# Kernel tuning notes

Hardware: AMD Instinct MI355X
Metric: run time of the kernel (lower is better)

## Reference

```python
import jax, jax.numpy as jnp
import numpy as np

HIDDEN = 2048
NUM_HEADS = 16
HEAD_DIM = 128
WINDOW = 1024
ROPE_THETA = 10000.0
B, L = 1, 4096


def setup_inputs() -> dict:
    key = jax.random.key(0)
    k0, k1, k2, k3, k4 = jax.random.split(key, 5)
    s = 1.0 / np.sqrt(HIDDEN)
    return {
        "hidden_states": jax.random.normal(k0, (B, L, HIDDEN), dtype=jnp.float32),
        "wq": jax.random.normal(k1, (HIDDEN, NUM_HEADS * HEAD_DIM), dtype=jnp.float32) * s,
        "wk": jax.random.normal(k2, (HIDDEN, NUM_HEADS * HEAD_DIM), dtype=jnp.float32) * s,
        "wv": jax.random.normal(k3, (HIDDEN, NUM_HEADS * HEAD_DIM), dtype=jnp.float32) * s,
        "wo": jax.random.normal(k4, (NUM_HEADS * HEAD_DIM, HIDDEN), dtype=jnp.float32) * s,
    }


def _apply_rotary(x, cos, sin):
    # x: [B, H, L, D]; cos/sin: [L, D/2]
    d2 = x.shape[-1] // 2
    x1, x2 = x[..., :d2], x[..., d2:]
    return jnp.concatenate([x1 * cos - x2 * sin, x2 * cos + x1 * sin], axis=-1)


def reference(hidden_states, wq, wk, wv, wo):
    Bsz, Ln, _ = hidden_states.shape
    dtype = hidden_states.dtype
    scale = HEAD_DIM ** (-0.5)

    def split_heads(x):
        return x.reshape(Bsz, Ln, NUM_HEADS, HEAD_DIM).transpose(0, 2, 1, 3)

    q = split_heads(hidden_states @ wq)
    k = split_heads(hidden_states @ wk)
    v = split_heads(hidden_states @ wv)

    inv_freq = 1.0 / (ROPE_THETA ** (jnp.arange(0, HEAD_DIM, 2, dtype=jnp.float32) / HEAD_DIM))
    pos = jnp.arange(Ln, dtype=jnp.float32)
    freqs = pos[:, None] * inv_freq[None, :]  # [L, D/2]
    cos = jnp.cos(freqs).astype(dtype)
    sin = jnp.sin(freqs).astype(dtype)

    q = _apply_rotary(q, cos, sin)
    k = _apply_rotary(k, cos, sin)

    q_pos = jnp.arange(Ln)[:, None]
    k_pos = jnp.arange(Ln)[None, :]
    valid = (k_pos > q_pos - WINDOW) & (k_pos <= q_pos)  # [L, L]
    neg = jnp.finfo(dtype).min

    attn = jnp.einsum("bhqd,bhkd->bhqk", q, k) * scale
    attn = jnp.where(valid, attn, neg)
    attn = jax.nn.softmax(attn, axis=-1)
    out = jnp.einsum("bhqk,bhkd->bhqd", attn, v)
    out = out.transpose(0, 2, 1, 3).reshape(Bsz, Ln, NUM_HEADS * HEAD_DIM)
    return out @ wo
```

## Files before the change

kernel.cpp:

```cpp
#include <hip/hip_runtime.h>
#include <cstdint>
#include <cstddef>

typedef unsigned short u16;
typedef __bf16 bf16x8 __attribute__((ext_vector_type(8)));
typedef float f32x4 __attribute__((ext_vector_type(4)));
typedef unsigned short u16x8 __attribute__((ext_vector_type(8)));

#define SEQ 4096
#define HID 2048
#define NH 16
#define HD 128
#define WIN 1024

__device__ __forceinline__ float bf2f(u16 u) {
  union { unsigned int i; float f; } v; v.i = ((unsigned int)u) << 16; return v.f;
}
__device__ __forceinline__ u16 f2bf(float f) {
  union { float f; unsigned int i; } v; v.f = f;
  unsigned int r = v.i + 0x7FFFu + ((v.i >> 16) & 1u);
  return (u16)(r >> 16);
}
__device__ __forceinline__ u16 f2bf_rne(float f) {
  union { __bf16 b; u16 u; } v; v.b = (__bf16)f; return v.u;
}
__device__ __forceinline__ unsigned pk2(float lo, float hi) {
  return (unsigned)f2bf_rne(lo) | ((unsigned)f2bf_rne(hi) << 16);
}
__device__ __forceinline__ float exp2a(float x) {
  float r; asm("v_exp_f32 %0, %1" : "=v"(r) : "v"(x)); return r;
}
template<int L2R>
__device__ __forceinline__ unsigned swz(unsigned o) { return o ^ (((o >> L2R) & 7u) << 4); }

__device__ __forceinline__ void gload_lds16(const u16* g, u16* l) {
  __builtin_amdgcn_global_load_lds((const __attribute__((address_space(1))) void*)g,
                                   (__attribute__((address_space(3))) void*)l, 16, 0, 0);
}


__global__ void cast_f32_bf16(const float* __restrict__ in, u16* __restrict__ out, int n4) {
  int i = blockIdx.x * blockDim.x + threadIdx.x;
  if (i < n4) {
    float4 v = ((const float4*)in)[i];
    union { u16 u[4]; unsigned long long ll; } r;
    r.u[0] = f2bf(v.x); r.u[1] = f2bf(v.y); r.u[2] = f2bf(v.z); r.u[3] = f2bf(v.w);
    ((unsigned long long*)out)[i] = r.ll;
  }
}

__global__ void transpose_cast4(const float* __restrict__ w0, const float* __restrict__ w1,
                                const float* __restrict__ w2, const float* __restrict__ w3,
                                u16* __restrict__ o0, u16* __restrict__ o1,
                                u16* __restrict__ o2, u16* __restrict__ o3) {
  __shared__ float t[32][33];
  const float* W = (blockIdx.z == 0) ? w0 : (blockIdx.z == 1) ? w1 : (blockIdx.z == 2) ? w2 : w3;
  u16* Wt = (blockIdx.z == 0) ? o0 : (blockIdx.z == 1) ? o1 : (blockIdx.z == 2) ? o2 : o3;
  const int tx = threadIdx.x & 31, ty = threadIdx.x >> 5;
  const int x0 = blockIdx.x * 32, y0 = blockIdx.y * 32;
#pragma unroll
  for (int i = 0; i < 4; ++i)
    t[ty + i * 8][tx] = W[(size_t)(y0 + ty + i * 8) * HID + x0 + tx];
  __syncthreads();
#pragma unroll
  for (int i = 0; i < 4; ++i)
    Wt[(size_t)(x0 + ty + i * 8) * HID + y0 + tx] = f2bf(t[tx][ty + i * 8]);
}

__global__ void rope_table(float* __restrict__ ctab, float* __restrict__ stab) {
  int idx = blockIdx.x * blockDim.x + threadIdx.x;
  int pos = idx >> 6, i = idx & 63;
  float invf = expf(-(float)i * 0.14391156831212787f);
  float ang = (float)pos * invf;
  float s, c;
  sincosf(ang, &s, &c);
  ctab[idx] = c; stab[idx] = s;
}


__global__ __launch_bounds__(256, 2) void gemm_qkv_kernel(
    const u16* __restrict__ X, const u16* __restrict__ Wqt, const u16* __restrict__ Wkt,
    const u16* __restrict__ Wvt, u16* __restrict__ Qo, u16* __restrict__ Ko, u16* __restrict__ Vo,
    const float* __restrict__ ctab, const float* __restrict__ stab) {
  __shared__ u16 ldsA[2][8192];
  __shared__ u16 ldsB[2][8192];
  int flat = (blockIdx.z * 32 + blockIdx.y) * 16 + blockIdx.x;
  int nf = (flat & 7) * 192 + (flat >> 3);
  int bx = nf & 15, by = (nf >> 4) & 31, bz = nf >> 9;
  const u16* Bt = (bz == 0) ? Wqt : (bz == 1) ? Wkt : Wvt;
  u16* Cp = (bz == 0) ? Qo : (bz == 1) ? Ko : Vo;
  const int brow = by * 128, bcol = bx * 128;

  const int lane = threadIdx.x & 63;
  const int wv = threadIdx.x >> 6;
  const int g = lane >> 4, c = lane & 15;
  const int K = HID, N = HID;

  const f32x4 zero = {0.f, 0.f, 0.f, 0.f};
  f32x4 acc[2][8];
#pragma unroll
  for (int m = 0; m < 2; ++m)
#pragma unroll
    for (int n = 0; n < 8; ++n) acc[m][n] = zero;

  auto stage = [&](int buf, int kt) {
    const int k0 = kt * 64;
#pragma unroll
    for (int i = 0; i < 4; ++i) {
      unsigned o = ((unsigned)(wv * 4 + i) * 64 + (unsigned)lane) * 16u;
      unsigned r = o >> 7;
      unsigned cb = swz<7>(o) & 127u;
      const size_t gcol = (size_t)k0 + (cb >> 1);
      gload_lds16(X + (size_t)(brow + r) * K + gcol, &ldsA[buf][(wv * 4 + i) * 512]);
      gload_lds16(Bt + (size_t)(bcol + r) * K + gcol, &ldsB[buf][(wv * 4 + i) * 512]);
    }
  };

  stage(0, 0);
  __syncthreads();
  int buf = 0;
  const int nt = K / 64;
  for (int kt = 0; kt < nt; ++kt) {
    if (kt + 1 < nt) stage(buf ^ 1, kt + 1);
    __builtin_amdgcn_s_setprio(1);
#pragma unroll
    for (int s = 0; s < 2; ++s) {
      const unsigned kb = (unsigned)(s * 64 + g * 16);
      bf16x8 af[2], bfv[8];
#pragma unroll
      for (int m = 0; m < 2; ++m) {
        unsigned row = wv * 32 + m * 16 + c;
        af[m] = *(const bf16x8*)((const char*)&ldsA[buf][0] + swz<7>(row * 128 + kb));
      }
#pragma unroll
      for (int n = 0; n < 8; ++n) {
        unsigned row = n * 16 + c;
        bfv[n] = *(const bf16x8*)((const char*)&ldsB[buf][0] + swz<7>(row * 128 + kb));
      }
#pragma unroll
      for (int m = 0; m < 2; ++m)
#pragma unroll
        for (int n = 0; n < 8; ++n)
          acc[m][n] = __builtin_amdgcn_mfma_f32_16x16x32_bf16(af[m], bfv[n], acc[m][n], 0, 0, 0);
    }
    __builtin_amdgcn_s_setprio(0);
    __syncthreads();
    buf ^= 1;
  }

  if (bz < 2) {
#pragma unroll
    for (int m = 0; m < 2; ++m) {
      const int rbase = brow + wv * 32 + m * 16 + g * 4;
#pragma unroll
      for (int r = 0; r < 4; ++r) {
        const int pos = rbase + r;
        const float* cp = ctab + (size_t)pos * 64;
        const float* sp = stab + (size_t)pos * 64;
        u16* crow = Cp + (size_t)pos * N + bcol;
#pragma unroll
        for (int n = 0; n < 4; ++n) {
          const int i = n * 16 + c;
          const float x1 = acc[m][n][r], x2 = acc[m][n + 4][r];
          const float co = cp[i], si = sp[i];
          crow[i] = f2bf(x1 * co - x2 * si);
          crow[i + 64] = f2bf(x2 * co + x1 * si);
        }
      }
    }
  } else {
#pragma unroll
    for (int m = 0; m < 2; ++m) {
      const int rbase = brow + wv * 32 + m * 16 + g * 4;
#pragma unroll
      for (int r = 0; r < 4; ++r) {
        u16* crow = Cp + (size_t)(rbase + r) * N + bcol;
#pragma unroll
        for (int n = 0; n < 8; ++n)
          crow[n * 16 + c] = f2bf(acc[m][n][r]);
      }
    }
  }
}


__global__ __launch_bounds__(256, 2) void gemm_out_kernel(
    const u16* __restrict__ Ob, const u16* __restrict__ Wot, float* __restrict__ out) {
  __shared__ u16 ldsA[2][8192];
  __shared__ u16 ldsB[2][8192];
  int flat = blockIdx.y * 16 + blockIdx.x;
  int nf = (flat & 7) * 64 + (flat >> 3);
  int bx = nf & 15, by = nf >> 4;
  const int brow = by * 128, bcol = bx * 128;

  const int lane = threadIdx.x & 63;
  const int wv = threadIdx.x >> 6;
  const int wr = wv >> 1, wc = wv & 1;
  const int g = lane >> 4, c = lane & 15;
  const int K = HID, N = HID;

  const f32x4 zero = {0.f, 0.f, 0.f, 0.f};
  f32x4 acc[4][4];
#pragma unroll
  for (int m = 0; m < 4; ++m)
#pragma unroll
    for (int n = 0; n < 4; ++n) acc[m][n] = zero;

  auto stage = [&](int buf, int kt) {
    const int k0 = kt * 64;
#pragma unroll
    for (int i = 0; i < 4; ++i) {
      unsigned o = ((unsigned)(wv * 4 + i) * 64 + (unsigned)lane) * 16u;
      unsigned r = o >> 7;
      unsigned cb = swz<7>(o) & 127u;
      const size_t gcol = (size_t)k0 + (cb >> 1);
      gload_lds16(Ob + (size_t)(brow + r) * K + gcol, &ldsA[buf][(wv * 4 + i) * 512]);
      gload_lds16(Wot + (size_t)(bcol + r) * K + gcol, &ldsB[buf][(wv * 4 + i) * 512]);
    }
  };

  stage(0, 0);
  __syncthreads();
  int buf = 0;
  const int nt = K / 64;
  for (int kt = 0; kt < nt; ++kt) {
    if (kt + 1 < nt) stage(buf ^ 1, kt + 1);
    __builtin_amdgcn_s_setprio(1);
#pragma unroll
    for (int s = 0; s < 2; ++s) {
      const unsigned kb = (unsigned)(s * 64 + g * 16);
      bf16x8 af[4], bfv[4];
#pragma unroll
      for (int m = 0; m < 4; ++m) {
        unsigned row = wr * 64 + m * 16 + c;
        af[m] = *(const bf16x8*)((const char*)&ldsA[buf][0] + swz<7>(row * 128 + kb));
      }
#pragma unroll
      for (int n = 0; n < 4; ++n) {
        unsigned row = wc * 64 + n * 16 + c;
        bfv[n] = *(const bf16x8*)((const char*)&ldsB[buf][0] + swz<7>(row * 128 + kb));
      }
#pragma unroll
      for (int m = 0; m < 4; ++m)
#pragma unroll
        for (int n = 0; n < 4; ++n)
          acc[m][n] = __builtin_amdgcn_mfma_f32_16x16x32_bf16(af[m], bfv[n], acc[m][n], 0, 0, 0);
    }
    __builtin_amdgcn_s_setprio(0);
    __syncthreads();
    buf ^= 1;
  }

#pragma unroll
  for (int m = 0; m < 4; ++m) {
    const int rbase = brow + wr * 64 + m * 16 + g * 4;
#pragma unroll
    for (int n = 0; n < 4; ++n) {
      const int cbase = bcol + wc * 64 + n * 16 + c;
#pragma unroll
      for (int r = 0; r < 4; ++r)
        out[(size_t)(rbase + r) * N + cbase] = acc[m][n][r];
    }
  }
}


__global__ __launch_bounds__(256, 3) void attn_kernel(
    const u16* __restrict__ Q, const u16* __restrict__ K,
    const u16* __restrict__ V, u16* __restrict__ O) {
  __shared__ u16 k_lds[2][8192];
  __shared__ u16 vt_lds[8192];

  const int lane = threadIdx.x & 63;
  const int wv = threadIdx.x >> 6;
  const int g = lane >> 4;
  const int c = lane & 15;

  int flat = blockIdx.y * 64 + blockIdx.x;
  int nf = (flat & 7) * 128 + (flat >> 3);
  const int q0 = (nf & 63) * 64;
  const int h = nf >> 6;
  const int qw = q0 + wv * 16;
  const int qpos = qw + c;

#pragma unroll
  for (int i = 0; i < 4; ++i) {
    unsigned o = ((unsigned)(wv * 4 + i) * 64 + (unsigned)lane) * 16u;
    unsigned r = o >> 8;
    unsigned cb = swz<8>(o) & 255u;
    gload_lds16(Q + (size_t)(q0 + r) * HID + h * HD + (cb >> 1), &k_lds[0][(wv * 4 + i) * 512]);
  }
  __syncthreads();
  bf16x8 qf[4];
#pragma unroll
  for (int s = 0; s < 4; ++s) {
    unsigned row = wv * 16 + c;
    qf[s] = *(const bf16x8*)((const char*)&k_lds[0][0] + swz<8>(row * 256 + s * 64 + g * 16));
  }
  __syncthreads();

  auto stageK = [&](int buf, int t0) {
#pragma unroll
    for (int i = 0; i < 4; ++i) {
      unsigned o = ((unsigned)(wv * 4 + i) * 64 + (unsigned)lane) * 16u;
      unsigned r = o >> 8;
      unsigned key = (r & 0x23u) | ((r & 0x0Cu) << 1) | ((r & 0x10u) >> 2);
      unsigned cb = swz<8>(o) & 255u;
      gload_lds16(K + (size_t)(t0 + (int)key) * HID + h * HD + (cb >> 1),
                  &k_lds[buf][(wv * 4 + i) * 512]);
    }
  };
  u16x8 vr[4];
  auto loadV = [&](int t0) {
    const u16x8* src = (const u16x8*)(V + (size_t)(t0 + lane) * HID + h * HD + wv * 32);
#pragma unroll
    for (int it = 0; it < 4; ++it) vr[it] = src[it];
  };
  auto writeVT = [&]() {
#pragma unroll
    for (int it = 0; it < 4; ++it)
#pragma unroll
      for (int j = 0; j < 8; ++j) {
        const int d = wv * 32 + it * 8 + j;
        vt_lds[d * 64 + (lane ^ ((d & 7) << 3))] = vr[it][j];
      }
  };

  const int t_start = (q0 >= WIN) ? (q0 - WIN) : 0;

  loadV(t_start);
  stageK(0, t_start);
  __syncthreads();
  writeVT();
  __syncthreads();

  const f32x4 zero = {0.f, 0.f, 0.f, 0.f};
  float mrow = -1e30f, lrow = 0.f;
  f32x4 oacc[8];
#pragma unroll
  for (int d = 0; d < 8; ++d) oacc[d] = zero;

  const float scale2 = 0.12751743f;
  int b = 0;

  for (int t0 = t_start; t0 <= q0; t0 += 64) {
    const bool has_next = (t0 + 64 <= q0);
    if (has_next) {
      loadV(t0 + 64);
      stageK(b ^ 1, t0 + 64);
    }

    f32x4 sa[4];
#pragma unroll
    for (int kf = 0; kf < 4; ++kf) sa[kf] = zero;
    __builtin_amdgcn_s_setprio(1);
#pragma unroll
    for (int s = 0; s < 4; ++s) {
#pragma unroll
      for (int kf = 0; kf < 4; ++kf) {
        unsigned row = kf * 16 + c;
        bf16x8 kb = *(const bf16x8*)((const char*)&k_lds[b][0] + swz<8>(row * 256 + s * 64 + g * 16));
        sa[kf] = __builtin_amdgcn_mfma_f32_16x16x32_bf16(kb, qf[s], sa[kf], 0, 0, 0);
      }
    }
    __builtin_amdgcn_s_setprio(0);

    const bool diag = (t0 == q0);
    const bool lowm = (q0 >= WIN) && (t0 == t_start);
    if (diag) {
#pragma unroll
      for (int kf = 0; kf < 4; ++kf) {
        const int kbase = t0 + (kf >> 1) * 32 + g * 8 + (kf & 1) * 4;
#pragma unroll
        for (int r = 0; r < 4; ++r) {
          float x = sa[kf][r] * scale2;
          sa[kf][r] = (kbase + r <= qpos) ? x : -1e30f;
        }
      }
    } else if (lowm) {
#pragma unroll
      for (int kf = 0; kf < 4; ++kf) {
        const int kbase = t0 + (kf >> 1) * 32 + g * 8 + (kf & 1) * 4;
#pragma unroll
        for (int r = 0; r < 4; ++r) {
          float x = sa[kf][r] * scale2;
          sa[kf][r] = (kbase + r > qpos - WIN) ? x : -1e30f;
        }
      }
    } else {
#pragma unroll
      for (int kf = 0; kf < 4; ++kf)
#pragma unroll
        for (int r = 0; r < 4; ++r) sa[kf][r] *= scale2;
    }

    float tmax = -3e38f;
#pragma unroll
    for (int kf = 0; kf < 4; ++kf)
#pragma unroll
      for (int r = 0; r < 4; ++r) tmax = fmaxf(tmax, sa[kf][r]);
    tmax = fmaxf(tmax, __shfl_xor(tmax, 16));
    tmax = fmaxf(tmax, __shfl_xor(tmax, 32));

    if (!__all((int)(tmax <= mrow + 8.f))) {
      const float mn = fmaxf(mrow, tmax);
      const float al = exp2a(mrow - mn);
      mrow = mn;
      lrow *= al;
      float alo[4];
#pragma unroll
      for (int r = 0; r < 4; ++r) alo[r] = __shfl(al, (lane & 48) | (g * 4 + r));
#pragma unroll
      for (int df = 0; df < 8; ++df)
#pragma unroll
        for (int r = 0; r < 4; ++r) oacc[df][r] *= alo[r];
    }

    float rs = 0.f;
    if (diag || lowm) {
#pragma unroll
      for (int kf = 0; kf < 4; ++kf)
#pragma unroll
        for (int r = 0; r < 4; ++r) {
          const float x = sa[kf][r];
          const float p = (x < -1e29f) ? 0.f : exp2a(x - mrow);
          sa[kf][r] = p; rs += p;
        }
    } else {
#pragma unroll
      for (int kf = 0; kf < 4; ++kf)
#pragma unroll
        for (int r = 0; r < 4; ++r) {
          const float p = exp2a(sa[kf][r] - mrow);
          sa[kf][r] = p; rs += p;
        }
    }
    rs += __shfl_xor(rs, 16);
    rs += __shfl_xor(rs, 32);
    lrow += rs;

    union { bf16x8 v; unsigned u[4]; } pa0, pa1;
    pa0.u[0] = pk2(sa[0][0], sa[0][1]); pa0.u[1] = pk2(sa[0][2], sa[0][3]);
    pa0.u[2] = pk2(sa[1][0], sa[1][1]); pa0.u[3] = pk2(sa[1][2], sa[1][3]);
    pa1.u[0] = pk2(sa[2][0], sa[2][1]); pa1.u[1] = pk2(sa[2][2], sa[2][3]);
    pa1.u[2] = pk2(sa[3][0], sa[3][1]); pa1.u[3] = pk2(sa[3][2], sa[3][3]);

    __builtin_amdgcn_s_setprio(1);
#pragma unroll
    for (int s2 = 0; s2 < 2; ++s2) {
      const bf16x8 pa = s2 ? pa1.v : pa0.v;
#pragma unroll
      for (int df = 0; df < 8; ++df) {
        const int row = df * 16 + c;
        const bf16x8 vb = *(const bf16x8*)&vt_lds[row * 64 + ((s2 * 32 + g * 8) ^ ((row & 7) << 3))];
        oacc[df] = __builtin_amdgcn_mfma_f32_16x16x32_bf16(pa, vb, oacc[df], 0, 0, 0);
      }
    }
    __builtin_amdgcn_s_setprio(0);

    asm volatile("s_waitcnt lgkmcnt(0)" ::: "memory");
    __builtin_amdgcn_s_barrier();

    if (has_next) {
      asm volatile("s_waitcnt vmcnt(4)" ::: "memory");
      writeVT();
    }
    asm volatile("s_waitcnt vmcnt(0) lgkmcnt(0)" ::: "memory");
    __builtin_amdgcn_s_barrier();
    b ^= 1;
  }

  float ilo[4];
  const float invl = 1.f / lrow;
#pragma unroll
  for (int r = 0; r < 4; ++r) ilo[r] = __shfl(invl, (lane & 48) | (g * 4 + r));
#pragma unroll
  for (int df = 0; df < 8; ++df)
#pragma unroll
    for (int r = 0; r < 4; ++r) {
      const int row = qw + g * 4 + r;
      const int col = h * HD + df * 16 + c;
      O[(size_t)row * HID + col] = f2bf(oacc[df][r] * ilo[r]);
    }
}


extern "C" void kernel_launch(void* const* d_in, const int* in_sizes, int n_in,
                              void* d_out, int out_size, void* d_ws, size_t ws_size,
                              hipStream_t stream) {
  const float* hidden = (const float*)d_in[0];
  const float* wq = (const float*)d_in[1];
  const float* wk = (const float*)d_in[2];
  const float* wv = (const float*)d_in[3];
  const float* wo = (const float*)d_in[4];
  float* out = (float*)d_out;

  char* ws = (char*)d_ws;
  u16* Xb  = (u16*)ws;                 ws += (size_t)SEQ * HID * 2;
  u16* Wqt = (u16*)ws;                 ws += (size_t)HID * HID * 2;
  u16* Wkt = (u16*)ws;                 ws += (size_t)HID * HID * 2;
  u16* Wvt = (u16*)ws;                 ws += (size_t)HID * HID * 2;
  u16* Wot = (u16*)ws;                 ws += (size_t)HID * HID * 2;
  u16* Qb  = (u16*)ws;                 ws += (size_t)SEQ * HID * 2;
  u16* Kb  = (u16*)ws;                 ws += (size_t)SEQ * HID * 2;
  u16* Vb  = (u16*)ws;                 ws += (size_t)SEQ * HID * 2;
  u16* Ob  = (u16*)ws;                 ws += (size_t)SEQ * HID * 2;
  float* ctab = (float*)ws;            ws += (size_t)SEQ * 64 * 4;
  float* stab = (float*)ws;            ws += (size_t)SEQ * 64 * 4;

  cast_f32_bf16<<<(SEQ * HID / 4 + 255) / 256, 256, 0, stream>>>(hidden, Xb, SEQ * HID / 4);

  dim3 tg(64, 64, 4);
  transpose_cast4<<<tg, 256, 0, stream>>>(wq, wk, wv, wo, Wqt, Wkt, Wvt, Wot);

  rope_table<<<(SEQ * 64) / 256, 256, 0, stream>>>(ctab, stab);

  dim3 gq(HID / 128, SEQ / 128, 3);
  gemm_qkv_kernel<<<gq, 256, 0, stream>>>(Xb, Wqt, Wkt, Wvt, Qb, Kb, Vb, ctab, stab);

  dim3 ga(SEQ / 64, NH);
  attn_kernel<<<ga, 256, 0, stream>>>(Qb, Kb, Vb, Ob);

  dim3 go(HID / 128, SEQ / 128);
  gemm_out_kernel<<<go, 256, 0, stream>>>(Ob, Wot, out);
}
```

Measured before the change: 265.2 us.

## Merge prep kernels into one launch and use 8-wave QKV GEMM blocks

Folds the hidden-state cast, the weight transpose-casts and the rope table generation into a single prep kernel launch to remove launch overhead. The QKV GEMM moves from 4 to 8 waves per block with a 2x4 wave grid, so each wave holds a 64x32 tile (4x2 MFMA accumulators) instead of 32x128. Each wave now owns matching rotary column pairs for the rope epilogue. This raises occupancy and cuts registers per wave, but each wave reuses fragments less and does more LDS reads per MFMA.

Measured after the change: 260.5 us. No clear change (-1.8%).

```diff
diff --git a/kernel.cpp b/kernel.cpp
--- a/kernel.cpp
+++ b/kernel.cpp
@@ -39,46 +39,53 @@
 }
 
 
-__global__ void cast_f32_bf16(const float* __restrict__ in, u16* __restrict__ out, int n4) {
-  int i = blockIdx.x * blockDim.x + threadIdx.x;
-  if (i < n4) {
-    float4 v = ((const float4*)in)[i];
-    union { u16 u[4]; unsigned long long ll; } r;
-    r.u[0] = f2bf(v.x); r.u[1] = f2bf(v.y); r.u[2] = f2bf(v.z); r.u[3] = f2bf(v.w);
-    ((unsigned long long*)out)[i] = r.ll;
-  }
-}
-
-__global__ void transpose_cast4(const float* __restrict__ w0, const float* __restrict__ w1,
-                                const float* __restrict__ w2, const float* __restrict__ w3,
-                                u16* __restrict__ o0, u16* __restrict__ o1,
-                                u16* __restrict__ o2, u16* __restrict__ o3) {
-  __shared__ float t[32][33];
-  const float* W = (blockIdx.z == 0) ? w0 : (blockIdx.z == 1) ? w1 : (blockIdx.z == 2) ? w2 : w3;
-  u16* Wt = (blockIdx.z == 0) ? o0 : (blockIdx.z == 1) ? o1 : (blockIdx.z == 2) ? o2 : o3;
-  const int tx = threadIdx.x & 31, ty = threadIdx.x >> 5;
-  const int x0 = blockIdx.x * 32, y0 = blockIdx.y * 32;
-#pragma unroll
-  for (int i = 0; i < 4; ++i)
-    t[ty + i * 8][tx] = W[(size_t)(y0 + ty + i * 8) * HID + x0 + tx];
-  __syncthreads();
-#pragma unroll
-  for (int i = 0; i < 4; ++i)
-    Wt[(size_t)(x0 + ty + i * 8) * HID + y0 + tx] = f2bf(t[tx][ty + i * 8]);
-}
-
-__global__ void rope_table(float* __restrict__ ctab, float* __restrict__ stab) {
-  int idx = blockIdx.x * blockDim.x + threadIdx.x;
-  int pos = idx >> 6, i = idx & 63;
-  float invf = expf(-(float)i * 0.14391156831212787f);
-  float ang = (float)pos * invf;
-  float s, c;
-  sincosf(ang, &s, &c);
-  ctab[idx] = c; stab[idx] = s;
-}
-
-
-__global__ __launch_bounds__(256, 2) void gemm_qkv_kernel(
+__global__ void prep_kernel(const float* __restrict__ hidden,
+                            const float* __restrict__ w0, const float* __restrict__ w1,
+                            const float* __restrict__ w2, const float* __restrict__ w3,
+                            u16* __restrict__ Xb,
+                            u16* __restrict__ o0, u16* __restrict__ o1,
+                            u16* __restrict__ o2, u16* __restrict__ o3,
+                            float* __restrict__ ctab, float* __restrict__ stab) {
+  const int z = blockIdx.z;
+  const int blk = blockIdx.y * 64 + blockIdx.x;
+  if (z == 0) {
+    int idx0 = blk * 256 + threadIdx.x;
+#pragma unroll
+    for (int t = 0; t < 2; ++t) {
+      int i = idx0 + t * (4096 * 256);
+      float4 v = ((const float4*)hidden)[i];
+      union { u16 u[4]; unsigned long long ll; } r;
+      r.u[0] = f2bf(v.x); r.u[1] = f2bf(v.y); r.u[2] = f2bf(v.z); r.u[3] = f2bf(v.w);
+      ((unsigned long long*)Xb)[i] = r.ll;
+    }
+  } else if (z <= 4) {
+    __shared__ float t[32][33];
+    const float* W = (z == 1) ? w0 : (z == 2) ? w1 : (z == 3) ? w2 : w3;
+    u16* Wt = (z == 1) ? o0 : (z == 2) ? o1 : (z == 3) ? o2 : o3;
+    const int tx = threadIdx.x & 31, ty = threadIdx.x >> 5;
+    const int x0 = blockIdx.x * 32, y0 = blockIdx.y * 32;
+#pragma unroll
+    for (int i = 0; i < 4; ++i)
+      t[ty + i * 8][tx] = W[(size_t)(y0 + ty + i * 8) * HID + x0 + tx];
+    __syncthreads();
+#pragma unroll
+    for (int i = 0; i < 4; ++i)
+      Wt[(size_t)(x0 + ty + i * 8) * HID + y0 + tx] = f2bf(t[tx][ty + i * 8]);
+  } else {
+    if (blk < 1024) {
+      int idx = blk * 256 + threadIdx.x;
+      int pos = idx >> 6, i = idx & 63;
+      float invf = expf(-(float)i * 0.14391156831212787f);
+      float ang = (float)pos * invf;
+      float s, c;
+      sincosf(ang, &s, &c);
+      ctab[idx] = c; stab[idx] = s;
+    }
+  }
+}
+
+
+__global__ __launch_bounds__(512, 4) void gemm_qkv_kernel(
     const u16* __restrict__ X, const u16* __restrict__ Wqt, const u16* __restrict__ Wkt,
     const u16* __restrict__ Wvt, u16* __restrict__ Qo, u16* __restrict__ Ko, u16* __restrict__ Vo,
     const float* __restrict__ ctab, const float* __restrict__ stab) {
@@ -91,28 +98,32 @@
   u16* Cp = (bz == 0) ? Qo : (bz == 1) ? Ko : Vo;
   const int brow = by * 128, bcol = bx * 128;
 
-  const int lane = threadIdx.x & 63;
-  const int wv = threadIdx.x >> 6;
+  const int tid = threadIdx.x;
+  const int lane = tid & 63;
+  const int wv = tid >> 6;
+  const int wr = wv >> 2;
+  const int wc = wv & 3;
   const int g = lane >> 4, c = lane & 15;
   const int K = HID, N = HID;
 
   const f32x4 zero = {0.f, 0.f, 0.f, 0.f};
-  f32x4 acc[2][8];
-#pragma unroll
-  for (int m = 0; m < 2; ++m)
-#pragma unroll
-    for (int n = 0; n < 8; ++n) acc[m][n] = zero;
+  f32x4 acc[4][2];
+#pragma unroll
+  for (int m = 0; m < 4; ++m)
+#pragma unroll
+    for (int j = 0; j < 2; ++j) acc[m][j] = zero;
 
   auto stage = [&](int buf, int kt) {
     const int k0 = kt * 64;
 #pragma unroll
-    for (int i = 0; i < 4; ++i) {
-      unsigned o = ((unsigned)(wv * 4 + i) * 64 + (unsigned)lane) * 16u;
+    for (int i = 0; i < 2; ++i) {
+      unsigned idx = (unsigned)(wv * 128 + i * 64 + lane);
+      unsigned o = idx * 16u;
       unsigned r = o >> 7;
       unsigned cb = swz<7>(o) & 127u;
       const size_t gcol = (size_t)k0 + (cb >> 1);
-      gload_lds16(X + (size_t)(brow + r) * K + gcol, &ldsA[buf][(wv * 4 + i) * 512]);
-      gload_lds16(Bt + (size_t)(bcol + r) * K + gcol, &ldsB[buf][(wv * 4 + i) * 512]);
+      gload_lds16(X + (size_t)(brow + r) * K + gcol, &ldsA[buf][idx * 8]);
+      gload_lds16(Bt + (size_t)(bcol + r) * K + gcol, &ldsB[buf][idx * 8]);
     }
   };
 
@@ -126,22 +137,22 @@
 #pragma unroll
     for (int s = 0; s < 2; ++s) {
       const unsigned kb = (unsigned)(s * 64 + g * 16);
-      bf16x8 af[2], bfv[8];
-#pragma unroll
-      for (int m = 0; m < 2; ++m) {
-        unsigned row = wv * 32 + m * 16 + c;
+      bf16x8 af[4], bfv[2];
+#pragma unroll
+      for (int m = 0; m < 4; ++m) {
+        unsigned row = (unsigned)(wr * 64 + m * 16 + c);
         af[m] = *(const bf16x8*)((const char*)&ldsA[buf][0] + swz<7>(row * 128 + kb));
       }
 #pragma unroll
-      for (int n = 0; n < 8; ++n) {
-        unsigned row = n * 16 + c;
-        bfv[n] = *(const bf16x8*)((const char*)&ldsB[buf][0] + swz<7>(row * 128 + kb));
-      }
-#pragma unroll
-      for (int m = 0; m < 2; ++m)
-#pragma unroll
-        for (int n = 0; n < 8; ++n)
-          acc[m][n] = __builtin_amdgcn_mfma_f32_16x16x32_bf16(af[m], bfv[n], acc[m][n], 0, 0, 0);
+      for (int j = 0; j < 2; ++j) {
+        unsigned row = (unsigned)((wc + j * 4) * 16 + c);
+        bfv[j] = *(const bf16x8*)((const char*)&ldsB[buf][0] + swz<7>(row * 128 + kb));
+      }
+#pragma unroll
+      for (int m = 0; m < 4; ++m)
+#pragma unroll
+        for (int j = 0; j < 2; ++j)
+          acc[m][j] = __builtin_amdgcn_mfma_f32_16x16x32_bf16(af[m], bfv[j], acc[m][j], 0, 0, 0);
     }
     __builtin_amdgcn_s_setprio(0);
     __syncthreads();
@@ -150,34 +161,29 @@
 
   if (bz < 2) {
 #pragma unroll
-    for (int m = 0; m < 2; ++m) {
-      const int rbase = brow + wv * 32 + m * 16 + g * 4;
+    for (int m = 0; m < 4; ++m) {
+      const int rbase = brow + wr * 64 + m * 16 + g * 4;
 #pragma unroll
       for (int r = 0; r < 4; ++r) {
         const int pos = rbase + r;
-        const float* cp = ctab + (size_t)pos * 64;
-        const float* sp = stab + (size_t)pos * 64;
+        const int i = wc * 16 + c;
+        const float co = ctab[(size_t)pos * 64 + i];
+        const float si = stab[(size_t)pos * 64 + i];
         u16* crow = Cp + (size_t)pos * N + bcol;
-#pragma unroll
-        for (int n = 0; n < 4; ++n) {
-          const int i = n * 16 + c;
-          const float x1 = acc[m][n][r], x2 = acc[m][n + 4][r];
-          const float co = cp[i], si = sp[i];
-          crow[i] = f2bf(x1 * co - x2 * si);
-          crow[i + 64] = f2bf(x2 * co + x1 * si);
-        }
+        const float x1 = acc[m][0][r], x2 = acc[m][1][r];
+        crow[i] = f2bf(x1 * co - x2 * si);
+        crow[i + 64] = f2bf(x2 * co + x1 * si);
       }
     }
   } else {
 #pragma unroll
-    for (int m = 0; m < 2; ++m) {
-      const int rbase = brow + wv * 32 + m * 16 + g * 4;
+    for (int m = 0; m < 4; ++m) {
+      const int rbase = brow + wr * 64 + m * 16 + g * 4;
 #pragma unroll
       for (int r = 0; r < 4; ++r) {
         u16* crow = Cp + (size_t)(rbase + r) * N + bcol;
-#pragma unroll
-        for (int n = 0; n < 8; ++n)
-          crow[n * 16 + c] = f2bf(acc[m][n][r]);
+        crow[wc * 16 + c] = f2bf(acc[m][0][r]);
+        crow[wc * 16 + 64 + c] = f2bf(acc[m][1][r]);
       }
     }
   }
@@ -508,15 +514,11 @@
   float* ctab = (float*)ws;            ws += (size_t)SEQ * 64 * 4;
   float* stab = (float*)ws;            ws += (size_t)SEQ * 64 * 4;
 
-  cast_f32_bf16<<<(SEQ * HID / 4 + 255) / 256, 256, 0, stream>>>(hidden, Xb, SEQ * HID / 4);
-
-  dim3 tg(64, 64, 4);
-  transpose_cast4<<<tg, 256, 0, stream>>>(wq, wk, wv, wo, Wqt, Wkt, Wvt, Wot);
-
-  rope_table<<<(SEQ * 64) / 256, 256, 0, stream>>>(ctab, stab);
+  dim3 gp(64, 64, 6);
+  prep_kernel<<<gp, 256, 0, stream>>>(hidden, wq, wk, wv, wo, Xb, Wqt, Wkt, Wvt, Wot, ctab, stab);
 
   dim3 gq(HID / 128, SEQ / 128, 3);
-  gemm_qkv_kernel<<<gq, 256, 0, stream>>>(Xb, Wqt, Wkt, Wvt, Qb, Kb, Vb, ctab, stab);
+  gemm_qkv_kernel<<<gq, 512, 0, stream>>>(Xb, Wqt, Wkt, Wvt, Qb, Kb, Vb, ctab, stab);
 
   dim3 ga(SEQ / 64, NH);
   attn_kernel<<<ga, 256, 0, stream>>>(Qb, Kb, Vb, Ob);
```
